# Performance work log

Hardware: AMD Instinct MI355X
Metric: run time of the kernel (lower is better)

## Reference

```python
import jax, jax.numpy as jnp
import numpy as np

N, D = 8192, 128


def setup_inputs() -> dict:
    key = jax.random.key(0)
    k1, k2 = jax.random.split(key)
    emb = jax.random.normal(k1, (N, D), dtype=jnp.float32)
    graphWeight = jax.random.uniform(k2, (N, N), dtype=jnp.float32)
    return {"emb": emb, "graphWeight": graphWeight}


def _pairwise_l2(x):
    # cdist(x, x, p=2) via the ||a-b||^2 = ||a||^2 + ||b||^2 - 2 a.b identity.
    sq_norms = jnp.sum(x * x, axis=-1)  # [N]
    sq = sq_norms[:, None] + sq_norms[None, :] - 2.0 * (x @ x.T)  # [N, N]
    sq = jnp.maximum(sq, 0.0)
    # safe sqrt (grad-safe at exactly-zero distances, e.g. the diagonal)
    return jnp.where(sq > 0.0, jnp.sqrt(jnp.where(sq > 0.0, sq, 1.0)), 0.0)


def reference(emb, graphWeight):
    dist = _pairwise_l2(emb)                 # [N, N]
    dist = dist / jnp.max(dist)              # normalize by global max
    return jnp.mean((1.0 - dist) * graphWeight)  # scalar loss
```

## Files before the change

### kernel.cpp

```cpp
#include <hip/hip_runtime.h>
#include <hip/hip_bf16.h>

#define NN 8192
#define DD 128
#define JTPB 16

typedef __attribute__((ext_vector_type(8))) short short8;
typedef __attribute__((ext_vector_type(4))) float f32x4;

__device__ __forceinline__ unsigned short f2bf(float x) {
    unsigned u = __float_as_uint(x);
    u += 0x7FFFu + ((u >> 16) & 1u);
    return (unsigned short)(u >> 16);
}
__device__ __forceinline__ float bf2f(unsigned short b) {
    return __uint_as_float(((unsigned)b) << 16);
}

__device__ __forceinline__ void gld_lds16(const float* src, float* ldst) {
    __builtin_amdgcn_global_load_lds(
        (const __attribute__((address_space(1))) void*)src,
        (__attribute__((address_space(3))) void*)ldst, 16, 0, 0);
}

__global__ void prep_kernel(const float* __restrict__ emb,
                            unsigned short* __restrict__ ebf,
                            float* __restrict__ nrm) {
    int row  = blockIdx.x * 4 + (threadIdx.x >> 6);
    int lane = threadIdx.x & 63;
    const float2 v = *reinterpret_cast<const float2*>(emb + (size_t)row * DD + lane * 2);
    unsigned short b0 = f2bf(v.x), b1 = f2bf(v.y);
    ushort2 st; st.x = b0; st.y = b1;
    *reinterpret_cast<ushort2*>(ebf + (size_t)row * DD + lane * 2) = st;
    float f0 = bf2f(b0), f1 = bf2f(b1);
    float s = f0 * f0 + f1 * f1;
    #pragma unroll
    for (int m = 32; m; m >>= 1) s += __shfl_xor(s, m);
    if (lane == 0) nrm[row] = s;
}

__global__ __launch_bounds__(256, 4)
void gram_kernel(const unsigned short* __restrict__ ebf,
                 const float* __restrict__ nrm,
                 const float* __restrict__ W,
                 float4* __restrict__ part) {
    __shared__ float wlds[2][32 * 128];
    __shared__ float sw_s[4], sdw_s[4], dm_s[4];

    const int wave = threadIdx.x >> 6;
    const int lane = threadIdx.x & 63;
    const int i0  = blockIdx.y * 128;
    const int iw  = i0 + wave * 32;
    const int jc0 = blockIdx.x * (JTPB * 32);

    const int lr = lane & 15;
    const int hi = lane >> 4;
    const int lk = hi * 8;

    int pj[4], pc[4];
    #pragma unroll
    for (int r = 0; r < 4; ++r) {
        int q = r * 256 + (int)threadIdx.x;
        pj[r] = q >> 5;
        pc[r] = ((q & 31) ^ (pj[r] & 7)) * 4;
    }

    short8 af[4][2];
    #pragma unroll
    for (int kc = 0; kc < 4; ++kc)
        #pragma unroll
        for (int m = 0; m < 2; ++m)
            af[kc][m] = *reinterpret_cast<const short8*>(
                ebf + (size_t)(iw + m * 16 + lr) * DD + kc * 32 + lk);
    f32x4 ni4[2];
    #pragma unroll
    for (int m = 0; m < 2; ++m)
        ni4[m] = *reinterpret_cast<const f32x4*>(nrm + iw + m * 16 + hi * 4);

    __builtin_amdgcn_sched_barrier(0);
    #pragma unroll
    for (int r = 0; r < 4; ++r)
        gld_lds16(W + (size_t)(jc0 + pj[r]) * NN + i0 + pc[r],
                  &wlds[0][r * 1024 + wave * 256]);
    __syncthreads();

    float sW = 0.f, sDW = 0.f, dmax = 0.f;

    for (int t = 0; t < JTPB; ++t) {
        const int jw = jc0 + t * 32;
        const int cb = t & 1;

        short8 bf[4][2];
        #pragma unroll
        for (int kc = 0; kc < 4; ++kc)
            #pragma unroll
            for (int n = 0; n < 2; ++n)
                bf[kc][n] = *reinterpret_cast<const short8*>(
                    ebf + (size_t)(jw + n * 16 + lr) * DD + kc * 32 + lk);
        float nj[2];
        #pragma unroll
        for (int n = 0; n < 2; ++n) nj[n] = nrm[jw + n * 16 + lr];

        __builtin_amdgcn_sched_barrier(0);
        if (t + 1 < JTPB) {
            #pragma unroll
            for (int r = 0; r < 4; ++r)
                gld_lds16(W + (size_t)(jw + 32 + pj[r]) * NN + i0 + pc[r],
                          &wlds[cb ^ 1][r * 1024 + wave * 256]);
        }
        __builtin_amdgcn_sched_barrier(0);

        f32x4 acc[2][2];
        #pragma unroll
        for (int m = 0; m < 2; ++m)
            #pragma unroll
            for (int n = 0; n < 2; ++n) acc[m][n] = (f32x4){0.f, 0.f, 0.f, 0.f};
        #pragma unroll
        for (int kc = 0; kc < 4; ++kc)
            #pragma unroll
            for (int m = 0; m < 2; ++m)
                #pragma unroll
                for (int n = 0; n < 2; ++n)
                    acc[m][n] = __builtin_amdgcn_mfma_f32_16x16x32_bf16(
                        af[kc][m], bf[kc][n], acc[m][n], 0, 0, 0);

        #pragma unroll
        for (int m = 0; m < 2; ++m) {
            #pragma unroll
            for (int n = 0; n < 2; ++n) {
                const int jp = n * 16 + lr;
                const int ck = (wave * 8 + m * 4 + hi) ^ (jp & 7);
                const f32x4 w4 = *reinterpret_cast<const f32x4*>(
                    &wlds[cb][jp * 128 + ck * 4]);
                #pragma unroll
                for (int r = 0; r < 4; ++r) {
                    float sq = ni4[m][r] + nj[n] - 2.0f * acc[m][n][r];
                    sq = fmaxf(sq, 0.0f);
                    float d = sqrtf(sq);
                    sW  += w4[r];
                    sDW += w4[r] * d;
                    dmax = fmaxf(dmax, d);
                }
            }
        }
        __syncthreads();
    }

    #pragma unroll
    for (int m = 32; m; m >>= 1) {
        sW  += __shfl_xor(sW, m);
        sDW += __shfl_xor(sDW, m);
        dmax = fmaxf(dmax, __shfl_xor(dmax, m));
    }
    if (lane == 0) { sw_s[wave] = sW; sdw_s[wave] = sDW; dm_s[wave] = dmax; }
    __syncthreads();
    if (threadIdx.x == 0) {
        float SW = 0.f, SDW = 0.f, DM = 0.f;
        #pragma unroll
        for (int k = 0; k < 4; ++k) {
            SW += sw_s[k]; SDW += sdw_s[k]; DM = fmaxf(DM, dm_s[k]);
        }
        float4 p; p.x = SW; p.y = SDW; p.z = DM; p.w = 0.f;
        part[blockIdx.y * gridDim.x + blockIdx.x] = p;
    }
}

__global__ __launch_bounds__(512)
void reduce_kernel(const float4* __restrict__ part, int nblk,
                   float* __restrict__ out) {
    const int tid = threadIdx.x;
    double sW = 0.0, sDW = 0.0;
    float dmax = 0.f;
    for (int idx = tid; idx < nblk; idx += 512) {
        float4 p = part[idx];
        sW += (double)p.x; sDW += (double)p.y; dmax = fmaxf(dmax, p.z);
    }
    #pragma unroll
    for (int m = 32; m; m >>= 1) {
        sW  += __shfl_xor(sW, m);
        sDW += __shfl_xor(sDW, m);
        dmax = fmaxf(dmax, __shfl_xor(dmax, m));
    }
    __shared__ double sw_s[8], sdw_s[8];
    __shared__ float dm_s[8];
    const int w = tid >> 6, l = tid & 63;
    if (l == 0) { sw_s[w] = sW; sdw_s[w] = sDW; dm_s[w] = dmax; }
    __syncthreads();
    if (tid == 0) {
        double SW = 0.0, SDW = 0.0; float DM = 0.f;
        #pragma unroll
        for (int k = 0; k < 8; ++k) {
            SW += sw_s[k]; SDW += sdw_s[k]; DM = fmaxf(DM, dm_s[k]);
        }
        out[0] = (float)((SW - SDW / (double)DM) / ((double)NN * (double)NN));
    }
}

extern "C" void kernel_launch(void* const* d_in, const int* in_sizes, int n_in,
                              void* d_out, int out_size, void* d_ws, size_t ws_size,
                              hipStream_t stream) {
    const float* emb = (const float*)d_in[0];
    const float* W   = (const float*)d_in[1];
    float* out = (float*)d_out;

    char* ws = (char*)d_ws;
    float4* part        = (float4*)ws;
    unsigned short* ebf = (unsigned short*)(ws + 32768);
    float* nrm          = (float*)(ws + 32768 + (size_t)NN * DD * 2);

    prep_kernel<<<NN / 4, 256, 0, stream>>>(emb, ebf, nrm);
    dim3 grid(NN / (32 * JTPB), NN / 128);
    gram_kernel<<<grid, 256, 0, stream>>>(ebf, nrm, W, part);
    reduce_kernel<<<1, 512, 0, stream>>>(part, grid.x * grid.y, out);
}
```

Before: 95.36 us.

## Restructure gram kernel into per-wave triple-buffered W pipeline without block barriers

Each wave now stages its own 16x32 slice of graphWeight into a private triple-buffered LDS region with direct global-to-LDS loads. It synchronises only with explicit vmcnt waits, so the per-iteration __syncthreads is gone. The B fragments of emb are register double-buffered and prefetched during the MFMA of the current tile. The j tile per step shrinks to 16 rows, the grid is remapped so blockIdx.x indexes i, and launch bounds drop to 3 waves per SIMD. The aim is to overlap W streaming with compute and remove block-wide barriers. The risk is that the hand-counted vmcnt values must match the compiler's outstanding loads.

```diff
diff --git a/kernel.cpp b/kernel.cpp
--- a/kernel.cpp
+++ b/kernel.cpp
@@ -3,7 +3,8 @@
 
 #define NN 8192
 #define DD 128
-#define JTPB 16
+#define JT 16
+#define JR 16
 
 typedef __attribute__((ext_vector_type(8))) short short8;
 typedef __attribute__((ext_vector_type(4))) float f32x4;
@@ -39,31 +40,25 @@
     if (lane == 0) nrm[row] = s;
 }
 
-__global__ __launch_bounds__(256, 4)
+__global__ __launch_bounds__(256, 3)
 void gram_kernel(const unsigned short* __restrict__ ebf,
                  const float* __restrict__ nrm,
                  const float* __restrict__ W,
                  float4* __restrict__ part) {
-    __shared__ float wlds[2][32 * 128];
+    __shared__ float wlds[4][3][JR * 32];
     __shared__ float sw_s[4], sdw_s[4], dm_s[4];
 
     const int wave = threadIdx.x >> 6;
     const int lane = threadIdx.x & 63;
-    const int i0  = blockIdx.y * 128;
-    const int iw  = i0 + wave * 32;
-    const int jc0 = blockIdx.x * (JTPB * 32);
-
     const int lr = lane & 15;
     const int hi = lane >> 4;
-    const int lk = hi * 8;
-
-    int pj[4], pc[4];
-    #pragma unroll
-    for (int r = 0; r < 4; ++r) {
-        int q = r * 256 + (int)threadIdx.x;
-        pj[r] = q >> 5;
-        pc[r] = ((q & 31) ^ (pj[r] & 7)) * 4;
-    }
+
+    const int i0w = blockIdx.x * 128 + wave * 32;
+    const int j0  = blockIdx.y * 256;
+
+    const int srow = lane >> 3;
+    const int schk = (lane & 7) ^ srow;
+    const float* wsrc = W + (size_t)(j0 + srow) * NN + i0w + schk * 4;
 
     short8 af[4][2];
     #pragma unroll
@@ -71,79 +66,81 @@
         #pragma unroll
         for (int m = 0; m < 2; ++m)
             af[kc][m] = *reinterpret_cast<const short8*>(
-                ebf + (size_t)(iw + m * 16 + lr) * DD + kc * 32 + lk);
+                ebf + (size_t)(i0w + m * 16 + lr) * DD + kc * 32 + hi * 8);
     f32x4 ni4[2];
     #pragma unroll
     for (int m = 0; m < 2; ++m)
-        ni4[m] = *reinterpret_cast<const f32x4*>(nrm + iw + m * 16 + hi * 4);
-
+        ni4[m] = *reinterpret_cast<const f32x4*>(nrm + i0w + m * 16 + hi * 4);
+
+    auto stage = [&](int t, int buf) {
+        float* dst = &wlds[wave][buf][0];
+        const float* s = wsrc + (size_t)t * JR * NN;
+        gld_lds16(s, dst);
+        gld_lds16(s + 8 * NN, dst + 256);
+    };
+    auto loadbf = [&](int t, short8 (&bf)[4], float& nj) {
+        const int jr = j0 + t * JR + lr;
+        #pragma unroll
+        for (int kc = 0; kc < 4; ++kc)
+            bf[kc] = *reinterpret_cast<const short8*>(
+                ebf + (size_t)jr * DD + kc * 32 + hi * 8);
+        nj = nrm[jr];
+    };
+
+    short8 bfA[4], bfB[4];
+    float njA = 0.f, njB = 0.f;
+    float sW = 0.f, sDW = 0.f, dmax = 0.f;
+
+    stage(0, 0);
     __builtin_amdgcn_sched_barrier(0);
-    #pragma unroll
-    for (int r = 0; r < 4; ++r)
-        gld_lds16(W + (size_t)(jc0 + pj[r]) * NN + i0 + pc[r],
-                  &wlds[0][r * 1024 + wave * 256]);
-    __syncthreads();
-
-    float sW = 0.f, sDW = 0.f, dmax = 0.f;
-
-    for (int t = 0; t < JTPB; ++t) {
-        const int jw = jc0 + t * 32;
-        const int cb = t & 1;
-
-        short8 bf[4][2];
-        #pragma unroll
-        for (int kc = 0; kc < 4; ++kc)
-            #pragma unroll
-            for (int n = 0; n < 2; ++n)
-                bf[kc][n] = *reinterpret_cast<const short8*>(
-                    ebf + (size_t)(jw + n * 16 + lr) * DD + kc * 32 + lk);
-        float nj[2];
-        #pragma unroll
-        for (int n = 0; n < 2; ++n) nj[n] = nrm[jw + n * 16 + lr];
-
-        __builtin_amdgcn_sched_barrier(0);
-        if (t + 1 < JTPB) {
-            #pragma unroll
-            for (int r = 0; r < 4; ++r)
-                gld_lds16(W + (size_t)(jw + 32 + pj[r]) * NN + i0 + pc[r],
-                          &wlds[cb ^ 1][r * 1024 + wave * 256]);
-        }
-        __builtin_amdgcn_sched_barrier(0);
-
-        f32x4 acc[2][2];
+    loadbf(0, bfA, njA);
+    __builtin_amdgcn_sched_barrier(0);
+    stage(1, 1);
+    __builtin_amdgcn_sched_barrier(0);
+
+    auto doTile = [&](int t, short8 (&bfc)[4], float& njc,
+                      short8 (&bfn)[4], float& njn) {
+        if (t < JT - 1) asm volatile("s_waitcnt vmcnt(2)" ::: "memory");
+        else            asm volatile("s_waitcnt vmcnt(0)" ::: "memory");
+        __builtin_amdgcn_sched_barrier(0);
+
+        const float* lb = &wlds[wave][t % 3][0];
+        f32x4 w4[2];
         #pragma unroll
         for (int m = 0; m < 2; ++m)
-            #pragma unroll
-            for (int n = 0; n < 2; ++n) acc[m][n] = (f32x4){0.f, 0.f, 0.f, 0.f};
+            w4[m] = *reinterpret_cast<const f32x4*>(
+                lb + lr * 32 + (((m * 4 + hi) ^ (lr & 7)) * 4));
+        __builtin_amdgcn_sched_barrier(0);
+
+        f32x4 acc[2] = {(f32x4){0.f,0.f,0.f,0.f}, (f32x4){0.f,0.f,0.f,0.f}};
         #pragma unroll
         for (int kc = 0; kc < 4; ++kc)
             #pragma unroll
             for (int m = 0; m < 2; ++m)
-                #pragma unroll
-                for (int n = 0; n < 2; ++n)
-                    acc[m][n] = __builtin_amdgcn_mfma_f32_16x16x32_bf16(
-                        af[kc][m], bf[kc][n], acc[m][n], 0, 0, 0);
-
-        #pragma unroll
-        for (int m = 0; m < 2; ++m) {
+                acc[m] = __builtin_amdgcn_mfma_f32_16x16x32_bf16(
+                    af[kc][m], bfc[kc], acc[m], 0, 0, 0);
+
+        if (t + 1 < JT) loadbf(t + 1, bfn, njn);
+        __builtin_amdgcn_sched_barrier(0);
+        if (t + 2 < JT) stage(t + 2, (t + 2) % 3);
+        __builtin_amdgcn_sched_barrier(0);
+
+        #pragma unroll
+        for (int m = 0; m < 2; ++m)
             #pragma unroll
-            for (int n = 0; n < 2; ++n) {
-                const int jp = n * 16 + lr;
-                const int ck = (wave * 8 + m * 4 + hi) ^ (jp & 7);
-                const f32x4 w4 = *reinterpret_cast<const f32x4*>(
-                    &wlds[cb][jp * 128 + ck * 4]);
-                #pragma unroll
-                for (int r = 0; r < 4; ++r) {
-                    float sq = ni4[m][r] + nj[n] - 2.0f * acc[m][n][r];
-                    sq = fmaxf(sq, 0.0f);
-                    float d = sqrtf(sq);
-                    sW  += w4[r];
-                    sDW += w4[r] * d;
-                    dmax = fmaxf(dmax, d);
-                }
+            for (int r = 0; r < 4; ++r) {
+                float sq = ni4[m][r] + njc - 2.0f * acc[m][r];
+                float d = sqrtf(fmaxf(sq, 0.0f));
+                sW  += w4[m][r];
+                sDW += w4[m][r] * d;
+                dmax = fmaxf(dmax, d);
             }
-        }
-        __syncthreads();
+    };
+
+    #pragma unroll
+    for (int t = 0; t < JT; t += 2) {
+        doTile(t,     bfA, njA, bfB, njB);
+        doTile(t + 1, bfB, njB, bfA, njA);
     }
 
     #pragma unroll
@@ -205,11 +202,11 @@
 
     char* ws = (char*)d_ws;
     float4* part        = (float4*)ws;
-    unsigned short* ebf = (unsigned short*)(ws + 32768);
-    float* nrm          = (float*)(ws + 32768 + (size_t)NN * DD * 2);
+    unsigned short* ebf = (unsigned short*)(ws + 65536);
+    float* nrm          = (float*)(ws + 65536 + (size_t)NN * DD * 2);
 
     prep_kernel<<<NN / 4, 256, 0, stream>>>(emb, ebf, nrm);
-    dim3 grid(NN / (32 * JTPB), NN / 128);
+    dim3 grid(NN / 128, NN / 256);
     gram_kernel<<<grid, 256, 0, stream>>>(ebf, nrm, W, part);
     reduce_kernel<<<1, 512, 0, stream>>>(part, grid.x * grid.y, out);
 }
```

Result: faster. 89.27 us (-6.4%).
